# Kernel tuning notes

Measured on AMD Instinct MI355X. Metric: run time of the kernel, lower is better.

## Reference

```python
import jax, jax.numpy as jnp
import numpy as np

N = 100000          # nodes
E = 1600000         # edges per adjacency (avg degree 16)
DIMS = [256, 128, 64]
ALPHA = 0.8
WD = 1e-4


def setup_inputs() -> dict:
    key = jax.random.key(0)
    ks = jax.random.split(key, 11)
    X = jax.random.normal(ks[0], (N, DIMS[0]), jnp.float32)
    rows = jax.random.randint(ks[1], (E,), 0, N, jnp.int32)
    cols = jax.random.randint(ks[2], (E,), 0, N, jnp.int32)
    prune_rows = jax.random.randint(ks[3], (E,), 0, N, jnp.int32)
    prune_cols = jax.random.randint(ks[4], (E,), 0, N, jnp.int32)
    # learned params (torch.randn init, scaled 0.1 for fp32 numeric headroom)
    W0 = jax.random.normal(ks[5], (DIMS[0], DIMS[1]), jnp.float32) * 0.1
    W1 = jax.random.normal(ks[6], (DIMS[1], DIMS[2]), jnp.float32) * 0.1
    v00 = jax.random.normal(ks[7], (DIMS[1], 1), jnp.float32) * 0.1
    v01 = jax.random.normal(ks[8], (DIMS[1], 1), jnp.float32) * 0.1
    pv00 = jax.random.normal(ks[9], (DIMS[1], 1), jnp.float32) * 0.1
    pv01 = jax.random.normal(ks[10], (DIMS[1], 1), jnp.float32) * 0.1
    return {"X": X, "W0": W0, "W1": W1, "v00": v00, "v01": v01,
            "pv00": pv00, "pv01": pv01, "rows": rows, "cols": cols,
            "prune_rows": prune_rows, "prune_cols": prune_cols}


def _edge_softmax(rows, logits, n):
    # row-wise softmax over sparse edge logits
    m = jax.ops.segment_max(logits, rows, num_segments=n)
    e = jnp.exp(logits - m[rows])
    s = jax.ops.segment_sum(e, rows, num_segments=n)
    return e / s[rows]


def _attention(rows, cols, H, va, vb, n):
    # logit_e = (H @ va)[src_e] + (H @ vb)[dst_e]  (binary adjacency values)
    f1 = (H @ va)[:, 0]
    f2 = (H @ vb)[:, 0]
    return _edge_softmax(rows, f1[rows] + f2[cols], n)


def _spmm(rows, cols, vals, H, n):
    # out[i] = sum_{e: rows[e]==i} vals[e] * H[cols[e]]
    return jax.ops.segment_sum(vals[:, None] * H[cols], rows, num_segments=n)


def reference(X, W0, W1, v00, v01, pv00, pv01, rows, cols, prune_rows, prune_cols):
    n = X.shape[0]
    # ---- encoder ----
    H1 = X @ W0                                   # layer 0 projection
    c = _attention(rows, cols, H1, v00, v01, n)   # C[0]
    pc = _attention(prune_rows, prune_cols, H1, pv00, pv01, n)  # prune_C[0]
    H1a = (1.0 - ALPHA) * _spmm(rows, cols, c, H1, n) \
        + ALPHA * _spmm(prune_rows, prune_cols, pc, H1, n)
    H1a = jax.nn.elu(H1a)                         # nonlinear, layer 0 != last
    H_enc = H1a @ W1                              # layer 1 == last: no attention
    # ---- decoder ----
    D = H_enc @ W1.T                              # layer 1
    D = (1.0 - ALPHA) * _spmm(rows, cols, c, D, n) \
        + ALPHA * _spmm(prune_rows, prune_cols, pc, D, n)
    D = jax.nn.elu(D)                             # nonlinear, layer 1 != 0
    X_ = D @ W0.T                                 # layer 0: plain matmul
    # ---- loss ----
    loss = jnp.sqrt(jnp.sum((X - X_) ** 2)) \
         + WD * (jnp.sum(W0 ** 2) + jnp.sum(W1 ** 2))
    return (loss, H_enc, X_)
```

## Files before the change

kernel.cpp:

```cpp
#include <hip/hip_runtime.h>
#include <math.h>

#define N_NODES 100000
#define N_EDGES 1600000
#define TOT (2 * N_NODES)
#define SCAN_NB 256
#define SCAN_CH 4
#define RPB 25000

static inline int cdiv(long a, long b) { return (int)((a + b - 1) / b); }

typedef unsigned int uint;
typedef unsigned short ushort;
typedef __attribute__((ext_vector_type(8))) short short8v;
typedef __attribute__((ext_vector_type(4))) float f32x4;

__device__ inline float bf2f(uint u) { return __uint_as_float(u << 16); }
__device__ inline ushort f2bf(float f) {
    uint u = __float_as_uint(f);
    uint r = ((u >> 16) & 1u) + 0x7fffu;
    return (ushort)((u + r) >> 16);
}

template <int K, int M, bool AF32, int OUT, bool ELU, bool LOSS>
__global__ __launch_bounds__(256) void gemm_mfma(const void* __restrict__ Av,
                                                 const ushort* __restrict__ Bcm,
                                                 void* __restrict__ Cv,
                                                 void* __restrict__ Cv2,
                                                 const float* __restrict__ Xref,
                                                 float* __restrict__ partial,
                                                 int nrows) {
    constexpr int BM = 128;
    constexpr int KP = K + 8;
    constexpr int NCT = M / 16;
    __shared__ ushort Blds[M * KP];
    __shared__ ushort Alds[BM * 32];
    const int w = threadIdx.x >> 6;
    const int l = threadIdx.x & 63;
    const int rowg = l & 15;
    const int kg = l >> 4;
    const int rbase = blockIdx.x * BM;
    {
        const uint4* src = reinterpret_cast<const uint4*>(Bcm);
        uint4* dst = reinterpret_cast<uint4*>(Blds);
        const int total = M * KP / 8;
        for (int i = threadIdx.x; i < total; i += 256) dst[i] = src[i];
    }
    f32x4 acc[2][NCT] = {};
    for (int k0 = 0; k0 < K; k0 += 32) {
        __syncthreads();
        int r = threadIdx.x >> 1;
        int kk = (threadIdx.x & 1) * 16;
        int rg = min(rbase + r, nrows - 1);
        if (AF32) {
            const float* A = (const float*)Av;
            const float4* src = reinterpret_cast<const float4*>(A + (size_t)rg * K + k0 + kk);
            ushort* dst = &Alds[r * 32 + kk];
#pragma unroll
            for (int q = 0; q < 4; ++q) {
                float4 v = src[q];
                dst[4 * q + 0] = f2bf(v.x); dst[4 * q + 1] = f2bf(v.y);
                dst[4 * q + 2] = f2bf(v.z); dst[4 * q + 3] = f2bf(v.w);
            }
        } else {
            const ushort* A = (const ushort*)Av;
            const uint4* src = reinterpret_cast<const uint4*>(A + (size_t)rg * K + k0 + kk);
            uint4* dst = reinterpret_cast<uint4*>(&Alds[r * 32 + kk]);
            dst[0] = src[0];
            dst[1] = src[1];
        }
        __syncthreads();
#pragma unroll
        for (int rt = 0; rt < 2; ++rt) {
            short8v af = *reinterpret_cast<const short8v*>(
                &Alds[(w * 32 + rt * 16 + rowg) * 32 + kg * 8]);
#pragma unroll
            for (int ct = 0; ct < NCT; ++ct) {
                short8v bf = *reinterpret_cast<const short8v*>(
                    &Blds[(ct * 16 + rowg) * KP + k0 + kg * 8]);
                acc[rt][ct] = __builtin_amdgcn_mfma_f32_16x16x32_bf16(
                    af, bf, acc[rt][ct], 0, 0, 0);
            }
        }
    }
    float lsum = 0.f;
#pragma unroll
    for (int rt = 0; rt < 2; ++rt) {
#pragma unroll
        for (int q = 0; q < 4; ++q) {
            int r = rbase + w * 32 + rt * 16 + kg * 4 + q;
            if (r >= nrows) continue;
#pragma unroll
            for (int ct = 0; ct < NCT; ++ct) {
                float o = acc[rt][ct][q];
                if (ELU) o = o > 0.f ? o : expm1f(o);
                int col = ct * 16 + rowg;
                if (OUT == 0 || OUT == 3) ((float*)Cv)[(size_t)r * M + col] = o;
                if (OUT == 2) ((ushort*)Cv)[(size_t)r * M + col] = f2bf(o);
                if (OUT == 3) ((ushort*)Cv2)[(size_t)r * M + col] = f2bf(o);
                if (LOSS) {
                    float d = o - Xref[(size_t)r * 256 + col];
                    lsum += d * d;
                }
            }
        }
    }
    if (LOSS) {
        __shared__ float smRed[4];
#pragma unroll
        for (int off = 32; off > 0; off >>= 1) lsum += __shfl_down(lsum, off);
        __syncthreads();
        if (l == 0) smRed[w] = lsum;
        __syncthreads();
        if (threadIdx.x == 0)
            partial[blockIdx.x] = smRed[0] + smRed[1] + smRed[2] + smRed[3];
    }
}

__global__ __launch_bounds__(256) void prep_all_kernel(const float* __restrict__ W0,
                                                       const float* __restrict__ W1,
                                                       ushort* __restrict__ B1,
                                                       ushort* __restrict__ B5,
                                                       ushort* __restrict__ B7,
                                                       ushort* __restrict__ B8) {
    int i = blockIdx.x * 256 + threadIdx.x;
    if (i < 32768) {
        int k = i / 128, m = i - k * 128;
        B1[m * 264 + k] = f2bf(W0[i]);
    } else if (i < 65536) {
        int j = i - 32768;
        int m = j / 128, k = j - m * 128;
        B8[m * 136 + k] = f2bf(W0[j]);
    } else if (i < 73728) {
        int j = i - 65536;
        int k = j / 64, m = j - k * 64;
        B5[m * 136 + k] = f2bf(W1[j]);
    } else if (i < 81920) {
        int j = i - 73728;
        int m = j / 64, k = j - m * 64;
        B7[m * 72 + k] = f2bf(W1[j]);
    }
}

__global__ __launch_bounds__(256) void attn_f4_kernel(const ushort* __restrict__ Hb,
                                                      const float* __restrict__ va,
                                                      const float* __restrict__ vb,
                                                      const float* __restrict__ pva,
                                                      const float* __restrict__ pvb,
                                                      float* __restrict__ f1,
                                                      float* __restrict__ f2,
                                                      float* __restrict__ pf1,
                                                      float* __restrict__ pf2) {
    int wid = (blockIdx.x * 256 + threadIdx.x) >> 6;
    int lane = threadIdx.x & 63;
    if (wid >= N_NODES) return;
    uint hv = reinterpret_cast<const uint*>(Hb + (size_t)wid * 128)[lane];
    float x0 = bf2f(hv & 0xffffu);
    float x1 = bf2f(hv >> 16);
    int k = 2 * lane;
    float a = x0 * va[k] + x1 * va[k + 1];
    float b = x0 * vb[k] + x1 * vb[k + 1];
    float pa = x0 * pva[k] + x1 * pva[k + 1];
    float pb = x0 * pvb[k] + x1 * pvb[k + 1];
#pragma unroll
    for (int off = 32; off > 0; off >>= 1) {
        a += __shfl_down(a, off);
        b += __shfl_down(b, off);
        pa += __shfl_down(pa, off);
        pb += __shfl_down(pb, off);
    }
    if (lane == 0) { f1[wid] = a; f2[wid] = b; pf1[wid] = pa; pf2[wid] = pb; }
}

__global__ __launch_bounds__(256) void hist2_kernel(const int* __restrict__ rows,
                                                    const int* __restrict__ prows,
                                                    int* __restrict__ deg) {
    int e = blockIdx.x * 256 + threadIdx.x;
    if (e >= 2 * N_EDGES) return;
    int b = e < N_EDGES ? rows[e] * 2 : prows[e - N_EDGES] * 2 + 1;
    atomicAdd(&deg[b], 1);
}

__device__ inline int pad8(int d) { return (d + 7) & ~7; }

__global__ __launch_bounds__(256) void scan1_kernel(const int* __restrict__ deg,
                                                    int* __restrict__ bsum) {
    __shared__ int sm[256];
    int base = (blockIdx.x * 256 + threadIdx.x) * SCAN_CH;
    int s = 0;
#pragma unroll
    for (int i = 0; i < SCAN_CH; ++i) {
        int idx = base + i;
        if (idx < TOT) s += pad8(deg[idx]);
    }
    sm[threadIdx.x] = s;
    __syncthreads();
    for (int off = 128; off > 0; off >>= 1) {
        if (threadIdx.x < off) sm[threadIdx.x] += sm[threadIdx.x + off];
        __syncthreads();
    }
    if (threadIdx.x == 0) bsum[blockIdx.x] = sm[0];
}

__global__ void scan2_kernel(int* __restrict__ bsum) {
    if (threadIdx.x != 0) return;
    int run = 0;
    for (int i = 0; i < SCAN_NB; ++i) {
        int t = bsum[i];
        bsum[i] = run;
        run += t;
    }
}

__global__ __launch_bounds__(256) void scan3_kernel(const int* __restrict__ deg,
                                                    const int* __restrict__ bsum,
                                                    int* __restrict__ rp) {
    __shared__ int sm[256];
    int base = (blockIdx.x * 256 + threadIdx.x) * SCAN_CH;
    int s = 0;
#pragma unroll
    for (int i = 0; i < SCAN_CH; ++i) {
        int idx = base + i;
        if (idx < TOT) s += pad8(deg[idx]);
    }
    sm[threadIdx.x] = s;
    __syncthreads();
    if (threadIdx.x == 0) {
        int run = bsum[blockIdx.x];
        for (int t = 0; t < 256; ++t) { int tmp = sm[t]; sm[t] = run; run += tmp; }
    }
    __syncthreads();
    int off = sm[threadIdx.x];
#pragma unroll
    for (int i = 0; i < SCAN_CH; ++i) {
        int idx = base + i;
        if (idx < TOT) { rp[idx] = off; off += pad8(deg[idx]); }
        else if (idx == TOT) rp[idx] = off;
    }
}

__global__ __launch_bounds__(256) void scatter_bucket_kernel(const int* __restrict__ rlist,
                                                             const int* __restrict__ clist,
                                                             int adj, int lo, int hi,
                                                             const int* __restrict__ rp,
                                                             int* __restrict__ cur,
                                                             int* __restrict__ ccol) {
    int e = blockIdx.x * 256 + threadIdx.x;
    if (e >= N_EDGES) return;
    int r0 = rlist[e];
    if (r0 < lo || r0 >= hi) return;
    int b = r0 * 2 + adj;
    int pos = rp[b] + atomicAdd(&cur[b], 1);
    ccol[pos] = clist[e];
}

__global__ __launch_bounds__(256) void edgeval_kernel(const int* __restrict__ rp,
                                                      const int* __restrict__ deg,
                                                      const int* __restrict__ ccol,
                                                      const float* __restrict__ f1,
                                                      const float* __restrict__ f2,
                                                      const float* __restrict__ pf1,
                                                      const float* __restrict__ pf2,
                                                      int2* __restrict__ eg) {
    int b = blockIdx.x * 16 + (threadIdx.x >> 4);
    int sl = threadIdx.x & 15;
    int adj = b & 1, r = b >> 1;
    float f1r = adj ? pf1[r] : f1[r];
    const float* f2t = adj ? pf2 : f2;
    float scale = adj ? 0.8f : 0.2f;
    int j0 = rp[b];
    int realend = j0 + deg[b];
    int pend = rp[b + 1];
    float s = 0.f;
    for (int j = j0 + sl; j < realend; j += 16)
        s += __expf(f1r + f2t[ccol[j]]);
#pragma unroll
    for (int off = 8; off > 0; off >>= 1) s += __shfl_xor(s, off);
    float inv = s > 0.f ? scale / s : 0.f;
    for (int j = j0 + sl; j < pend; j += 16) {
        if (j < realend) {
            int c = ccol[j];
            float wv = __expf(f1r + f2t[c]) * inv;
            eg[j] = make_int2(c, __float_as_int(wv));
        } else {
            eg[j] = make_int2(0, 0);
        }
    }
}

#define SPU 8
__global__ __launch_bounds__(256) void spmm_fused_kernel(const int* __restrict__ rp,
                                                         const int2* __restrict__ eg,
                                                         const ushort* __restrict__ Hb,
                                                         float* __restrict__ out) {
    int r = blockIdx.x * 4 + (threadIdx.x >> 6);
    int lane = threadIdx.x & 63;
    const uint* Hu = reinterpret_cast<const uint*>(Hb);
    float a0 = 0.f, a1 = 0.f;
    int j = rp[2 * r], E = rp[2 * r + 2];
    if (j < E) {
        int2 d[SPU]; uint h[SPU];
#pragma unroll
        for (int u = 0; u < SPU; ++u) d[u] = eg[j + u];
#pragma unroll
        for (int u = 0; u < SPU; ++u) h[u] = Hu[(uint)d[u].x * 64u + lane];
        j += SPU;
        for (; j < E; j += SPU) {
            int2 dn[SPU]; uint hn[SPU];
#pragma unroll
            for (int u = 0; u < SPU; ++u) dn[u] = eg[j + u];
#pragma unroll
            for (int u = 0; u < SPU; ++u) hn[u] = Hu[(uint)dn[u].x * 64u + lane];
#pragma unroll
            for (int u = 0; u < SPU; ++u) {
                float v = __int_as_float(d[u].y);
                a0 += v * bf2f(h[u] & 0xffffu);
                a1 += v * bf2f(h[u] >> 16);
            }
#pragma unroll
            for (int u = 0; u < SPU; ++u) { d[u] = dn[u]; h[u] = hn[u]; }
        }
#pragma unroll
        for (int u = 0; u < SPU; ++u) {
            float v = __int_as_float(d[u].y);
            a0 += v * bf2f(h[u] & 0xffffu);
            a1 += v * bf2f(h[u] >> 16);
        }
    }
    float o0 = a0 > 0.f ? a0 : expm1f(a0);
    float o1 = a1 > 0.f ? a1 : expm1f(a1);
    *reinterpret_cast<float2*>(out + (size_t)r * 128 + 2 * lane) = make_float2(o0, o1);
}

__global__ __launch_bounds__(256) void spmm64_fused_kernel(const int* __restrict__ rp,
                                                           const int2* __restrict__ eg,
                                                           const ushort* __restrict__ Hb,
                                                           ushort* __restrict__ Sh) {
    int r = blockIdx.x * 4 + (threadIdx.x >> 6);
    int lane = threadIdx.x & 63;
    float a = 0.f;
    int j = rp[2 * r], E = rp[2 * r + 2];
    if (j < E) {
        int2 d[SPU]; ushort h[SPU];
#pragma unroll
        for (int u = 0; u < SPU; ++u) d[u] = eg[j + u];
#pragma unroll
        for (int u = 0; u < SPU; ++u) h[u] = Hb[(uint)d[u].x * 64u + lane];
        j += SPU;
        for (; j < E; j += SPU) {
            int2 dn[SPU]; ushort hn[SPU];
#pragma unroll
            for (int u = 0; u < SPU; ++u) dn[u] = eg[j + u];
#pragma unroll
            for (int u = 0; u < SPU; ++u) hn[u] = Hb[(uint)dn[u].x * 64u + lane];
#pragma unroll
            for (int u = 0; u < SPU; ++u)
                a += __int_as_float(d[u].y) * bf2f((uint)h[u]);
#pragma unroll
            for (int u = 0; u < SPU; ++u) { d[u] = dn[u]; h[u] = hn[u]; }
        }
#pragma unroll
        for (int u = 0; u < SPU; ++u)
            a += __int_as_float(d[u].y) * bf2f((uint)h[u]);
    }
    Sh[(size_t)r * 64 + lane] = f2bf(a);
}

__global__ __launch_bounds__(256) void sq_reduce_kernel(const float* __restrict__ a,
                                                        float* __restrict__ acc, int n) {
    __shared__ float sm[4];
    float s = 0.f;
    for (int i = blockIdx.x * 256 + threadIdx.x; i < n; i += gridDim.x * 256) {
        float d = a[i];
        s += d * d;
    }
#pragma unroll
    for (int off = 32; off > 0; off >>= 1) s += __shfl_down(s, off);
    int lane = threadIdx.x & 63, w = threadIdx.x >> 6;
    if (lane == 0) sm[w] = s;
    __syncthreads();
    if (threadIdx.x == 0) atomicAdd(acc, sm[0] + sm[1] + sm[2] + sm[3]);
}

__global__ __launch_bounds__(256) void partial_reduce_kernel(const float* __restrict__ p,
                                                             int n, float* __restrict__ acc) {
    __shared__ float sm[4];
    float s = 0.f;
    for (int i = threadIdx.x; i < n; i += 256) s += p[i];
#pragma unroll
    for (int off = 32; off > 0; off >>= 1) s += __shfl_down(s, off);
    int lane = threadIdx.x & 63, w = threadIdx.x >> 6;
    if (lane == 0) sm[w] = s;
    __syncthreads();
    if (threadIdx.x == 0) atomicAdd(acc, sm[0] + sm[1] + sm[2] + sm[3]);
}

__global__ void finalize_kernel(const float* __restrict__ acc, float* __restrict__ out) {
    out[0] = sqrtf(acc[0]) + 1e-4f * acc[1];
}

extern "C" void kernel_launch(void* const* d_in, const int* in_sizes, int n_in,
                              void* d_out, int out_size, void* d_ws, size_t ws_size,
                              hipStream_t stream) {
    const float* X    = (const float*)d_in[0];
    const float* W0   = (const float*)d_in[1];
    const float* W1   = (const float*)d_in[2];
    const float* v00  = (const float*)d_in[3];
    const float* v01  = (const float*)d_in[4];
    const float* pv00 = (const float*)d_in[5];
    const float* pv01 = (const float*)d_in[6];
    const int* rows   = (const int*)d_in[7];
    const int* cols   = (const int*)d_in[8];
    const int* prows  = (const int*)d_in[9];
    const int* pcols  = (const int*)d_in[10];

    float* out  = (float*)d_out;
    float* Henc = out + 1;
    float* Xrec = out + 1 + (size_t)N_NODES * 64;

    ushort* bufAh  = (ushort*)(out + 6400004);
    ushort* Sh     = (ushort*)(out + 6400004);
    int*    ccol   = (int*)(out + 12800004);
    int2*   eg     = (int2*)(out + 17600004);
    ushort* HencB  = (ushort*)(out + 27200004);
    int*    deg    = (int*)(out + 28800004);
    int*    cur    = deg + TOT;

    float* ws   = (float*)d_ws;
    float* bufB = ws;
    ushort* bufBh = (ushort*)bufB;
    float* f1   = bufB + (size_t)N_NODES * 128;
    float* f2   = f1 + N_NODES;
    float* pf1  = f2 + N_NODES;
    float* pf2  = pf1 + N_NODES;
    float* acc  = pf2 + N_NODES;
    ushort* B1cm = (ushort*)(acc + 4);
    ushort* B5cm = B1cm + 128 * 264;
    ushort* B7cm = B5cm + 64 * 136;
    ushort* B8cm = B7cm + 128 * 72;
    int*   rp   = (int*)(B8cm + 256 * 136);
    int*   bsum = rp + TOT + 1;
    float* partial = (float*)(bsum + SCAN_NB);

    const int n = N_NODES;
    const int EG = cdiv(N_EDGES, 256);
    const int EG2 = cdiv(2 * (long)N_EDGES, 256);

    prep_all_kernel<<<cdiv(81920, 256), 256, 0, stream>>>(W0, W1, B1cm, B5cm, B7cm, B8cm);

    gemm_mfma<256, 128, true, 2, false, false><<<cdiv(n, 128), 256, 0, stream>>>(
        X, B1cm, bufAh, nullptr, nullptr, nullptr, n);

    hipMemsetAsync(deg, 0, 2 * (size_t)TOT * sizeof(int), stream);
    hipMemsetAsync(acc, 0, 4 * sizeof(float), stream);

    attn_f4_kernel<<<cdiv(n, 4), 256, 0, stream>>>(bufAh, v00, v01, pv00, pv01,
                                                   f1, f2, pf1, pf2);

    hist2_kernel<<<EG2, 256, 0, stream>>>(rows, prows, deg);
    scan1_kernel<<<SCAN_NB, 256, 0, stream>>>(deg, bsum);
    scan2_kernel<<<1, 64, 0, stream>>>(bsum);
    scan3_kernel<<<SCAN_NB, 256, 0, stream>>>(deg, bsum, rp);
    for (int p = 0; p < 4; ++p)
        scatter_bucket_kernel<<<EG, 256, 0, stream>>>(rows, cols, 0,
                                                      p * RPB, (p + 1) * RPB,
                                                      rp, cur, ccol);
    for (int p = 0; p < 4; ++p)
        scatter_bucket_kernel<<<EG, 256, 0, stream>>>(prows, pcols, 1,
                                                      p * RPB, (p + 1) * RPB,
                                                      rp, cur, ccol);
    edgeval_kernel<<<cdiv(TOT, 16), 256, 0, stream>>>(rp, deg, ccol,
                                                      f1, f2, pf1, pf2, eg);

    spmm_fused_kernel<<<n / 4, 256, 0, stream>>>(rp, eg, bufAh, bufB);

    gemm_mfma<128, 64, true, 3, false, false><<<cdiv(n, 128), 256, 0, stream>>>(
        bufB, B5cm, Henc, HencB, nullptr, nullptr, n);

    spmm64_fused_kernel<<<n / 4, 256, 0, stream>>>(rp, eg, HencB, Sh);

    gemm_mfma<64, 128, false, 2, true, false><<<cdiv(n, 128), 256, 0, stream>>>(
        Sh, B7cm, bufBh, nullptr, nullptr, nullptr, n);

    gemm_mfma<128, 256, false, 0, false, true><<<cdiv(n, 128), 256, 0, stream>>>(
        bufBh, B8cm, Xrec, nullptr, X, partial, n);

    partial_reduce_kernel<<<1, 256, 0, stream>>>(partial, cdiv(n, 128), acc + 0);
    sq_reduce_kernel<<<16, 256, 0, stream>>>(W0, acc + 1, 256 * 128);
    sq_reduce_kernel<<<4, 256, 0, stream>>>(W1, acc + 1, 128 * 64);
    finalize_kernel<<<1, 1, 0, stream>>>(acc, out);
}
```

Before: 794.2 us.

## Fuse attention logits into GEMM, drop scan2, unbucket scatter, bf16 spmm output

The attention-logit dot products are computed in the epilogue of the first GEMM from fp32 accumulators, which removes a separate pass over H1. The scan2 kernel is folded into scan3, where each block sums the preceding block totals. The bucketed scatter (eight launches) becomes two plain scatter launches, and the two weight-norm reductions are merged into one kernel. The first spmm now writes bf16 instead of fp32, which halves the traffic into the following GEMM. In exchange, logits now use fp32 values rather than bf16-rounded ones, and the unbucketed scatter loses the locality that the bucketing aimed to give.

After: 745.4 us. 1.07x faster.

```diff
diff --git a/kernel.cpp b/kernel.cpp
--- a/kernel.cpp
+++ b/kernel.cpp
@@ -6,7 +6,6 @@
 #define TOT (2 * N_NODES)
 #define SCAN_NB 256
 #define SCAN_CH 4
-#define RPB 25000
 
 static inline int cdiv(long a, long b) { return (int)((a + b - 1) / b); }
 
@@ -22,13 +21,21 @@
     return (ushort)((u + r) >> 16);
 }
 
-template <int K, int M, bool AF32, int OUT, bool ELU, bool LOSS>
+template <int K, int M, bool AF32, int OUT, bool ELU, bool LOSS, bool ATTN>
 __global__ __launch_bounds__(256) void gemm_mfma(const void* __restrict__ Av,
                                                  const ushort* __restrict__ Bcm,
                                                  void* __restrict__ Cv,
                                                  void* __restrict__ Cv2,
                                                  const float* __restrict__ Xref,
                                                  float* __restrict__ partial,
+                                                 const float* __restrict__ va,
+                                                 const float* __restrict__ vb,
+                                                 const float* __restrict__ pva,
+                                                 const float* __restrict__ pvb,
+                                                 float* __restrict__ f1,
+                                                 float* __restrict__ f2,
+                                                 float* __restrict__ pf1,
+                                                 float* __restrict__ pf2,
                                                  int nrows) {
     constexpr int BM = 128;
     constexpr int KP = K + 8;
@@ -101,6 +108,37 @@
                 if (LOSS) {
                     float d = o - Xref[(size_t)r * 256 + col];
                     lsum += d * d;
+                }
+            }
+        }
+    }
+    if (ATTN) {
+        float var[NCT], vbr[NCT], pvar[NCT], pvbr[NCT];
+#pragma unroll
+        for (int ct = 0; ct < NCT; ++ct) {
+            int col = ct * 16 + rowg;
+            var[ct] = va[col]; vbr[ct] = vb[col];
+            pvar[ct] = pva[col]; pvbr[ct] = pvb[col];
+        }
+#pragma unroll
+        for (int rt = 0; rt < 2; ++rt) {
+#pragma unroll
+            for (int q = 0; q < 4; ++q) {
+                int r = rbase + w * 32 + rt * 16 + kg * 4 + q;
+                float da = 0.f, db = 0.f, dpa = 0.f, dpb = 0.f;
+#pragma unroll
+                for (int ct = 0; ct < NCT; ++ct) {
+                    float o = acc[rt][ct][q];
+                    da += o * var[ct]; db += o * vbr[ct];
+                    dpa += o * pvar[ct]; dpb += o * pvbr[ct];
+                }
+#pragma unroll
+                for (int m = 1; m < 16; m <<= 1) {
+                    da += __shfl_xor(da, m); db += __shfl_xor(db, m);
+                    dpa += __shfl_xor(dpa, m); dpb += __shfl_xor(dpb, m);
+                }
+                if (rowg == 0 && r < nrows) {
+                    f1[r] = da; f2[r] = db; pf1[r] = dpa; pf2[r] = dpb;
                 }
             }
         }
@@ -142,36 +180,6 @@
     }
 }
 
-__global__ __launch_bounds__(256) void attn_f4_kernel(const ushort* __restrict__ Hb,
-                                                      const float* __restrict__ va,
-                                                      const float* __restrict__ vb,
-                                                      const float* __restrict__ pva,
-                                                      const float* __restrict__ pvb,
-                                                      float* __restrict__ f1,
-                                                      float* __restrict__ f2,
-                                                      float* __restrict__ pf1,
-                                                      float* __restrict__ pf2) {
-    int wid = (blockIdx.x * 256 + threadIdx.x) >> 6;
-    int lane = threadIdx.x & 63;
-    if (wid >= N_NODES) return;
-    uint hv = reinterpret_cast<const uint*>(Hb + (size_t)wid * 128)[lane];
-    float x0 = bf2f(hv & 0xffffu);
-    float x1 = bf2f(hv >> 16);
-    int k = 2 * lane;
-    float a = x0 * va[k] + x1 * va[k + 1];
-    float b = x0 * vb[k] + x1 * vb[k + 1];
-    float pa = x0 * pva[k] + x1 * pva[k + 1];
-    float pb = x0 * pvb[k] + x1 * pvb[k + 1];
-#pragma unroll
-    for (int off = 32; off > 0; off >>= 1) {
-        a += __shfl_down(a, off);
-        b += __shfl_down(b, off);
-        pa += __shfl_down(pa, off);
-        pb += __shfl_down(pb, off);
-    }
-    if (lane == 0) { f1[wid] = a; f2[wid] = b; pf1[wid] = pa; pf2[wid] = pb; }
-}
-
 __global__ __launch_bounds__(256) void hist2_kernel(const int* __restrict__ rows,
                                                     const int* __restrict__ prows,
                                                     int* __restrict__ deg) {
@@ -202,20 +210,16 @@
     if (threadIdx.x == 0) bsum[blockIdx.x] = sm[0];
 }
 
-__global__ void scan2_kernel(int* __restrict__ bsum) {
-    if (threadIdx.x != 0) return;
-    int run = 0;
-    for (int i = 0; i < SCAN_NB; ++i) {
-        int t = bsum[i];
-        bsum[i] = run;
-        run += t;
-    }
-}
-
 __global__ __launch_bounds__(256) void scan3_kernel(const int* __restrict__ deg,
                                                     const int* __restrict__ bsum,
                                                     int* __restrict__ rp) {
     __shared__ int sm[256];
+    __shared__ int base0;
+    if (threadIdx.x == 0) {
+        int run = 0;
+        for (int i = 0; i < blockIdx.x; ++i) run += bsum[i];
+        base0 = run;
+    }
     int base = (blockIdx.x * 256 + threadIdx.x) * SCAN_CH;
     int s = 0;
 #pragma unroll
@@ -226,7 +230,7 @@
     sm[threadIdx.x] = s;
     __syncthreads();
     if (threadIdx.x == 0) {
-        int run = bsum[blockIdx.x];
+        int run = base0;
         for (int t = 0; t < 256; ++t) { int tmp = sm[t]; sm[t] = run; run += tmp; }
     }
     __syncthreads();
@@ -239,17 +243,15 @@
     }
 }
 
-__global__ __launch_bounds__(256) void scatter_bucket_kernel(const int* __restrict__ rlist,
-                                                             const int* __restrict__ clist,
-                                                             int adj, int lo, int hi,
-                                                             const int* __restrict__ rp,
-                                                             int* __restrict__ cur,
-                                                             int* __restrict__ ccol) {
+__global__ __launch_bounds__(256) void scatter_kernel(const int* __restrict__ rlist,
+                                                      const int* __restrict__ clist,
+                                                      int adj,
+                                                      const int* __restrict__ rp,
+                                                      int* __restrict__ cur,
+                                                      int* __restrict__ ccol) {
     int e = blockIdx.x * 256 + threadIdx.x;
     if (e >= N_EDGES) return;
-    int r0 = rlist[e];
-    if (r0 < lo || r0 >= hi) return;
-    int b = r0 * 2 + adj;
+    int b = rlist[e] * 2 + adj;
     int pos = rp[b] + atomicAdd(&cur[b], 1);
     ccol[pos] = clist[e];
 }
@@ -292,7 +294,7 @@
 __global__ __launch_bounds__(256) void spmm_fused_kernel(const int* __restrict__ rp,
                                                          const int2* __restrict__ eg,
                                                          const ushort* __restrict__ Hb,
-                                                         float* __restrict__ out) {
+                                                         uint* __restrict__ outh) {
     int r = blockIdx.x * 4 + (threadIdx.x >> 6);
     int lane = threadIdx.x & 63;
     const uint* Hu = reinterpret_cast<const uint*>(Hb);
@@ -329,7 +331,7 @@
     }
     float o0 = a0 > 0.f ? a0 : expm1f(a0);
     float o1 = a1 > 0.f ? a1 : expm1f(a1);
-    *reinterpret_cast<float2*>(out + (size_t)r * 128 + 2 * lane) = make_float2(o0, o1);
+    outh[(size_t)r * 64 + lane] = (uint)f2bf(o0) | ((uint)f2bf(o1) << 16);
 }
 
 __global__ __launch_bounds__(256) void spmm64_fused_kernel(const int* __restrict__ rp,
@@ -366,12 +368,13 @@
     Sh[(size_t)r * 64 + lane] = f2bf(a);
 }
 
-__global__ __launch_bounds__(256) void sq_reduce_kernel(const float* __restrict__ a,
-                                                        float* __restrict__ acc, int n) {
+__global__ __launch_bounds__(256) void sqw_reduce_kernel(const float* __restrict__ W0,
+                                                         const float* __restrict__ W1,
+                                                         float* __restrict__ acc) {
     __shared__ float sm[4];
     float s = 0.f;
-    for (int i = blockIdx.x * 256 + threadIdx.x; i < n; i += gridDim.x * 256) {
-        float d = a[i];
+    for (int i = blockIdx.x * 256 + threadIdx.x; i < 40960; i += gridDim.x * 256) {
+        float d = i < 32768 ? W0[i] : W1[i - 32768];
         s += d * d;
     }
 #pragma unroll
@@ -427,9 +430,8 @@
     int*    cur    = deg + TOT;
 
     float* ws   = (float*)d_ws;
-    float* bufB = ws;
-    ushort* bufBh = (ushort*)bufB;
-    float* f1   = bufB + (size_t)N_NODES * 128;
+    ushort* bufBh = (ushort*)ws;
+    float* f1   = ws + (size_t)N_NODES * 128;
     float* f2   = f1 + N_NODES;
     float* pf1  = f2 + N_NODES;
     float* pf2  = pf1 + N_NODES;
@@ -448,45 +450,38 @@
 
     prep_all_kernel<<<cdiv(81920, 256), 256, 0, stream>>>(W0, W1, B1cm, B5cm, B7cm, B8cm);
 
-    gemm_mfma<256, 128, true, 2, false, false><<<cdiv(n, 128), 256, 0, stream>>>(
-        X, B1cm, bufAh, nullptr, nullptr, nullptr, n);
+    gemm_mfma<256, 128, true, 2, false, false, true><<<cdiv(n, 128), 256, 0, stream>>>(
+        X, B1cm, bufAh, nullptr, nullptr, nullptr,
+        v00, v01, pv00, pv01, f1, f2, pf1, pf2, n);
 
     hipMemsetAsync(deg, 0, 2 * (size_t)TOT * sizeof(int), stream);
     hipMemsetAsync(acc, 0, 4 * sizeof(float), stream);
 
-    attn_f4_kernel<<<cdiv(n, 4), 256, 0, stream>>>(bufAh, v00, v01, pv00, pv01,
-                                                   f1, f2, pf1, pf2);
-
     hist2_kernel<<<EG2, 256, 0, stream>>>(rows, prows, deg);
     scan1_kernel<<<SCAN_NB, 256, 0, stream>>>(deg, bsum);
-    scan2_kernel<<<1, 64, 0, stream>>>(bsum);
     scan3_kernel<<<SCAN_NB, 256, 0, stream>>>(deg, bsum, rp);
-    for (int p = 0; p < 4; ++p)
-        scatter_bucket_kernel<<<EG, 256, 0, stream>>>(rows, cols, 0,
-                                                      p * RPB, (p + 1) * RPB,
-                                                      rp, cur, ccol);
-    for (int p = 0; p < 4; ++p)
-        scatter_bucket_kernel<<<EG, 256, 0, stream>>>(prows, pcols, 1,
-                                                      p * RPB, (p + 1) * RPB,
-                                                      rp, cur, ccol);
+    scatter_kernel<<<EG, 256, 0, stream>>>(rows, cols, 0, rp, cur, ccol);
+    scatter_kernel<<<EG, 256, 0, stream>>>(prows, pcols, 1, rp, cur, ccol);
     edgeval_kernel<<<cdiv(TOT, 16), 256, 0, stream>>>(rp, deg, ccol,
                                                       f1, f2, pf1, pf2, eg);
 
-    spmm_fused_kernel<<<n / 4, 256, 0, stream>>>(rp, eg, bufAh, bufB);
-
-    gemm_mfma<128, 64, true, 3, false, false><<<cdiv(n, 128), 256, 0, stream>>>(
-        bufB, B5cm, Henc, HencB, nullptr, nullptr, n);
+    spmm_fused_kernel<<<n / 4, 256, 0, stream>>>(rp, eg, bufAh, (uint*)bufBh);
+
+    gemm_mfma<128, 64, false, 3, false, false, false><<<cdiv(n, 128), 256, 0, stream>>>(
+        bufBh, B5cm, Henc, HencB, nullptr, nullptr,
+        nullptr, nullptr, nullptr, nullptr, nullptr, nullptr, nullptr, nullptr, n);
 
     spmm64_fused_kernel<<<n / 4, 256, 0, stream>>>(rp, eg, HencB, Sh);
 
-    gemm_mfma<64, 128, false, 2, true, false><<<cdiv(n, 128), 256, 0, stream>>>(
-        Sh, B7cm, bufBh, nullptr, nullptr, nullptr, n);
-
-    gemm_mfma<128, 256, false, 0, false, true><<<cdiv(n, 128), 256, 0, stream>>>(
-        bufBh, B8cm, Xrec, nullptr, X, partial, n);
+    gemm_mfma<64, 128, false, 2, true, false, false><<<cdiv(n, 128), 256, 0, stream>>>(
+        Sh, B7cm, bufBh, nullptr, nullptr, nullptr,
+        nullptr, nullptr, nullptr, nullptr, nullptr, nullptr, nullptr, nullptr, n);
+
+    gemm_mfma<128, 256, false, 0, false, true, false><<<cdiv(n, 128), 256, 0, stream>>>(
+        bufBh, B8cm, Xrec, nullptr, X, partial,
+        nullptr, nullptr, nullptr, nullptr, nullptr, nullptr, nullptr, nullptr, n);
 
     partial_reduce_kernel<<<1, 256, 0, stream>>>(partial, cdiv(n, 128), acc + 0);
-    sq_reduce_kernel<<<16, 256, 0, stream>>>(W0, acc + 1, 256 * 128);
-    sq_reduce_kernel<<<4, 256, 0, stream>>>(W1, acc + 1, 128 * 64);
+    sqw_reduce_kernel<<<20, 256, 0, stream>>>(W0, W1, acc + 1);
     finalize_kernel<<<1, 1, 0, stream>>>(acc, out);
 }
```
